# Kernel tuning notes

Measured on AMD Instinct MI355X. Metric: run time of the kernel, lower is better.

## Reference

```python
import jax, jax.numpy as jnp
import numpy as np

NATOMS = 20000
NEDGES = 400000
EMB = 256
NUM_RBF = 50
NUM_GATES = 10
K = 2
FOUT = 128
BASE = 0.0
OUTER = 5.0


def setup_inputs() -> dict:
    key = jax.random.key(0)
    ks = jax.random.split(key, 24)
    z = jax.random.randint(ks[0], (NATOMS,), 0, 100, dtype=jnp.int32)
    pos = jax.random.normal(ks[1], (NATOMS, 3), jnp.float32)
    batch = jnp.zeros((NATOMS,), jnp.int32)
    edge_index = jax.random.randint(ks[2], (2, NEDGES), 0, NATOMS, dtype=jnp.int32)
    edge_weight = jax.random.uniform(ks[3], (NEDGES,), jnp.float32, 0.5, OUTER)
    edge_vec = jax.random.normal(ks[4], (NEDGES, 3), jnp.float32)
    noise = jax.random.normal(ks[5], (NEDGES, NUM_GATES), jnp.float32)
    # learned parameters (torch Linear stored pre-transposed as [in, out])
    emb = jax.random.normal(ks[6], (100, EMB), jnp.float32) * 0.1
    Wd = jax.random.normal(ks[7], (NUM_RBF, EMB), jnp.float32) * 0.05
    bd = jnp.zeros((EMB,), jnp.float32)
    Wdt = jax.random.normal(ks[8], (EMB, EMB), jnp.float32) * 0.05
    bdt = jnp.zeros((EMB,), jnp.float32)
    Wai = jax.random.normal(ks[9], (EMB, EMB), jnp.float32) * 0.05
    bai = jnp.zeros((EMB,), jnp.float32)
    Waj = jax.random.normal(ks[10], (EMB, EMB), jnp.float32) * 0.05
    baj = jnp.zeros((EMB,), jnp.float32)
    Wgam = jax.random.normal(ks[11], (3 * EMB, EMB), jnp.float32) * 0.03
    bgam = jnp.zeros((EMB,), jnp.float32)
    W_g = jax.random.normal(ks[12], (EMB, NUM_GATES), jnp.float32) * 0.01
    W_noise = jax.random.normal(ks[13], (EMB, NUM_GATES), jnp.float32) * 0.01
    W_exp = jax.random.normal(ks[14], (K, EMB, FOUT), jnp.float32) * 0.05
    b_exp = jnp.zeros((K, FOUT), jnp.float32)
    return dict(z=z, pos=pos, batch=batch, edge_index=edge_index,
                edge_weight=edge_weight, edge_vec=edge_vec, noise=noise,
                emb=emb, Wd=Wd, bd=bd, Wdt=Wdt, bdt=bdt, Wai=Wai, bai=bai,
                Waj=Waj, baj=baj, Wgam=Wgam, bgam=bgam, W_g=W_g,
                W_noise=W_noise, W_exp=W_exp, b_exp=b_exp)


def reference(z, pos, batch, edge_index, edge_weight, edge_vec, noise,
              emb, Wd, bd, Wdt, bdt, Wai, bai, Waj, baj, Wgam, bgam,
              W_g, W_noise, W_exp, b_exp):
    n_atoms = z.shape[0]
    src, dst = edge_index[0], edge_index[1]
    x = emb[z]                                              # [N, EMB]
    # Gaussian RBF expansion on [BASE, OUTER]
    offset = jnp.linspace(BASE, OUTER, NUM_RBF)
    coeff = -0.5 / (offset[1] - offset[0]) ** 2
    edge_attr = jnp.exp(coeff * (edge_weight[:, None] - offset) ** 2)  # [E, NUM_RBF]
    # Cosine cutoff (lower cutoff == 0 branch)
    C = 0.5 * (jnp.cos(edge_weight * (np.pi / OUTER)) + 1.0) * (edge_weight < OUTER)
    # normalized edge directions
    evn = edge_vec / jnp.linalg.norm(edge_vec, axis=1, keepdims=True)  # [E, 3]
    d_proj = (edge_attr @ Wd + bd) * C[:, None]             # [E, EMB]
    d_t = d_proj @ Wdt + bdt                                # [E, EMB]
    a_i = x[src] @ Wai + bai                                # [E, EMB]
    a_j = x[dst] @ Waj + baj                                # [E, EMB]
    gamma = jnp.concatenate([d_t, a_i, a_j], axis=1) @ Wgam + bgam  # [E, EMB]
    # noisy top-k gating
    H = d_t @ W_g + noise * jax.nn.softplus(d_t @ W_noise)  # [E, G]
    top_v, top_i = jax.lax.top_k(H, K)                      # [E, K]
    Hm = jnp.where(H >= top_v[:, -1:], H, -jnp.inf)
    gating = jax.nn.softmax(Hm, axis=-1)                    # [E, G]
    # quirk of the original: expert slot i always sees gamma, experts 0..K-1 used
    expert_out = jnp.einsum('ed,kdf->ekf', gamma, W_exp) + b_exp  # [E, K, FOUT]
    gate_w = jnp.take_along_axis(gating, top_i, axis=1)     # [E, K]
    edge_out = (expert_out * gate_w[:, :, None]).sum(axis=1)  # [E, FOUT]
    atom_out = jax.ops.segment_sum(edge_out, src, num_segments=n_atoms)  # [N, FOUT]
    vec = jax.ops.segment_sum(evn[:, :, None] * edge_out[:, None, :], src,
                              num_segments=n_atoms)         # [N, 3, FOUT]
    return atom_out, vec
```

## Files before the change

### kernel.cpp

```cpp
#include <hip/hip_runtime.h>
#include <math.h>

#define NATOMS 20000
#define NEDGES 400000
#define EMBD   256
#define NRBF   50
#define NGATE  10
#define FOUT   128
#define APB    4
#define OUTERC 5.0f

#define RBF_D    (5.0f/49.0f)
#define RBF_INVD (49.0f/5.0f)
#define RBF_C2   (-0.5f*(49.0f/5.0f)*(49.0f/5.0f)*1.4426950408889634f)
#define PI_OVER_OUTER 0.62831853071795864769f

static __device__ __forceinline__ float softplusf(float x){
    return (x > 15.0f) ? x : __logf(1.0f + __expf(x));
}
static __device__ __forceinline__ unsigned bfr(float v){
    unsigned u = __float_as_uint(v);
    return (u + 0x7fffu + ((u >> 16) & 1u)) & 0xffff0000u;
}
#define BLO(u) __uint_as_float((u) << 16)
#define BHI(u) __uint_as_float((u) & 0xffff0000u)

__global__ __launch_bounds__(256) void k_ag(
    const float* __restrict__ Wd, const float* __restrict__ Wdt,
    const float* __restrict__ bd, const float* __restrict__ bdt,
    const float* __restrict__ bgam, const float* __restrict__ Wgam,
    const float* __restrict__ Wexp, const float* __restrict__ bexp,
    const float* __restrict__ Wg, const float* __restrict__ Wn,
    const float* __restrict__ emb,
    const float* __restrict__ Wai, const float* __restrict__ bai,
    const float* __restrict__ Waj, const float* __restrict__ baj,
    const int* __restrict__ esrc, int* __restrict__ counts,
    float* __restrict__ R0, float* __restrict__ R1,
    float* __restrict__ Qg, float* __restrict__ Qn, float* __restrict__ sv,
    float* __restrict__ Ti0, float* __restrict__ Ti1,
    float* __restrict__ Tj0, float* __restrict__ Tj1)
{
    const int b = blockIdx.x, t = threadIdx.x;
    if (b >= 252) {
        int e = (b - 252) * 256 + t;
        if (e < NEDGES) atomicAdd(&counts[esrc[e]], 1);
        return;
    }
    __shared__ float ya[256], za[256];
    if (b >= 52) {
        const int side = (b >= 152);
        const int m = side ? b - 152 : b - 52;
        const float* er = emb + m*EMBD;
        const float* W1 = side ? Waj : Wai;
        const float* b1 = side ? baj : bai;
        float s = b1[t];
        #pragma unroll 8
        for (int k = 0; k < EMBD; k++) s += er[k] * W1[k*EMBD + t];
        ya[t] = s;
        __syncthreads();
        const float* G = Wgam + (size_t)(side ? 512 : 256) * EMBD;
        s = 0.f;
        #pragma unroll 8
        for (int k = 0; k < EMBD; k++) s += ya[k] * G[k*EMBD + t];
        za[t] = s;
        __syncthreads();
        const int half = t >> 7, ff = t & 127;
        const float* WX = Wexp + (size_t)half*EMBD*FOUT;
        s = 0.f;
        #pragma unroll 8
        for (int k = 0; k < EMBD; k++) s += za[k] * WX[k*FOUT + ff];
        float* dst = side ? (half ? Tj1 : Tj0) : (half ? Ti1 : Ti0);
        dst[m*FOUT + ff] = s;
        return;
    }
    const int m = b;
    float s;
    if (m < 50) {
        const float* wr = Wd + m*EMBD;
        s = 0.f;
        #pragma unroll 8
        for (int k = 0; k < EMBD; k++) s += wr[k] * Wdt[k*EMBD + t];
    } else if (m == 50) {
        s = 0.f;
        #pragma unroll 8
        for (int k = 0; k < EMBD; k++) s += bd[k] * Wdt[k*EMBD + t];
    } else {
        s = bdt[t];
    }
    ya[t] = s;
    __syncthreads();
    s = 0.f;
    #pragma unroll 8
    for (int k = 0; k < EMBD; k++) s += ya[k] * Wgam[k*EMBD + t];
    if (m == 51) s += bgam[t];
    za[t] = s;
    __syncthreads();
    const int half = t >> 7, ff = t & 127;
    const float* WX = Wexp + (size_t)half*EMBD*FOUT;
    s = 0.f;
    #pragma unroll 8
    for (int k = 0; k < EMBD; k++) s += za[k] * WX[k*FOUT + ff];
    if (m < 50)       (half ? R1 : R0)[m*FOUT + ff] = s;
    else if (m == 50) sv[half*FOUT + ff] = s;
    else              sv[256 + half*FOUT + ff] = s + bexp[half*FOUT + ff];
    if (t < 20) {
        const int tt = t % 10;
        const float* WT = (t < 10) ? Wg : Wn;
        float q = 0.f;
        #pragma unroll 8
        for (int k = 0; k < EMBD; k++) q += ya[k] * WT[k*NGATE + tt];
        if (m < 50) { float* Q = (t < 10) ? Qg : Qn; Q[m*12 + tt] = q; }
        else {
            int off = (m == 50) ? ((t < 10) ? 512 : 532) : ((t < 10) ? 522 : 542);
            sv[off + tt] = q;
            float* Q = (t < 10) ? Qg : Qn; Q[m*12 + tt] = 0.f;
        }
    }
}

__global__ __launch_bounds__(256) void k_scan(
    const int* __restrict__ counts, int* __restrict__ cursors)
{
    const int t = threadIdx.x;
    __shared__ int part[256];
    const int CH = (NATOMS + 255) / 256;
    int base = t * CH, s = 0;
    for (int i = 0; i < CH; i++) { int idx = base + i; if (idx < NATOMS) s += counts[idx]; }
    part[t] = s;
    __syncthreads();
    for (int d = 1; d < 256; d <<= 1) {
        int v = (t >= d) ? part[t - d] : 0;
        __syncthreads();
        part[t] += v;
        __syncthreads();
    }
    int run = (t == 0) ? 0 : part[t - 1];
    for (int i = 0; i < CH; i++) {
        int idx = base + i;
        if (idx < NATOMS) { cursors[idx] = run; run += counts[idx]; }
    }
}

__global__ __launch_bounds__(256) void k_edge(
    const int* __restrict__ z, const int* __restrict__ esrc, const int* __restrict__ edst,
    const float* __restrict__ ew, const float* __restrict__ evec, const float* __restrict__ noise,
    const float* __restrict__ Qg, const float* __restrict__ Qn, const float* __restrict__ sv,
    int* __restrict__ cursors,
    float4* __restrict__ rec, unsigned* __restrict__ zdj)
{
    __shared__ float qgL[52*12], qnL[52*12];
    __shared__ float nbuf[256*11];
    __shared__ float vbuf[768];
    const int t = threadIdx.x;
    const int e0 = blockIdx.x * 256;

    for (int i = t; i < 52*12; i += 256) { qgL[i] = Qg[i]; qnL[i] = Qn[i]; }
    #pragma unroll
    for (int q = 0; q < 10; q++) {
        int idx = q*256 + t; long long g = (long long)e0*10 + idx;
        if (g < (long long)NEDGES*10) { int r_ = idx/10; nbuf[r_*11 + (idx - r_*10)] = noise[g]; }
    }
    #pragma unroll
    for (int q = 0; q < 3; q++) {
        int idx = q*256 + t; long long g = (long long)e0*3 + idx;
        if (g < (long long)NEDGES*3) vbuf[idx] = evec[g];
    }
    __syncthreads();

    int e = e0 + t;
    if (e >= NEDGES) return;
    float w = ew[e];
    float C = (w < OUTERC) ? 0.5f*(__cosf(w*PI_OVER_OUTER) + 1.0f) : 0.0f;
    int iw = (int)(w * RBF_INVD);
    int j0 = (iw - 4) & ~3;
    j0 = max(0, min(40, j0));
    float rW[12];
    #pragma unroll
    for (int k = 0; k < 12; k++) { float tt = w - (j0+k)*RBF_D; rW[k] = exp2f(RBF_C2*tt*tt); }
    float hg[NGATE], hn[NGATE];
    #pragma unroll
    for (int g2 = 0; g2 < NGATE; g2++) { hg[g2] = 0.f; hn[g2] = 0.f; }
    #pragma unroll
    for (int k = 0; k < 12; k++) {
        float rk = rW[k];
        const float* qg = &qgL[(j0+k)*12];
        const float* qn = &qnL[(j0+k)*12];
        float4 ga = *(const float4*)qg; float4 gb = *(const float4*)(qg+4);
        float2 gc = *(const float2*)(qg+8);
        float4 na = *(const float4*)qn; float4 nb = *(const float4*)(qn+4);
        float2 nc = *(const float2*)(qn+8);
        hg[0]=fmaf(rk,ga.x,hg[0]); hg[1]=fmaf(rk,ga.y,hg[1]); hg[2]=fmaf(rk,ga.z,hg[2]); hg[3]=fmaf(rk,ga.w,hg[3]);
        hg[4]=fmaf(rk,gb.x,hg[4]); hg[5]=fmaf(rk,gb.y,hg[5]); hg[6]=fmaf(rk,gb.z,hg[6]); hg[7]=fmaf(rk,gb.w,hg[7]);
        hg[8]=fmaf(rk,gc.x,hg[8]); hg[9]=fmaf(rk,gc.y,hg[9]);
        hn[0]=fmaf(rk,na.x,hn[0]); hn[1]=fmaf(rk,na.y,hn[1]); hn[2]=fmaf(rk,na.z,hn[2]); hn[3]=fmaf(rk,na.w,hn[3]);
        hn[4]=fmaf(rk,nb.x,hn[4]); hn[5]=fmaf(rk,nb.y,hn[5]); hn[6]=fmaf(rk,nb.z,hn[6]); hn[7]=fmaf(rk,nb.w,hn[7]);
        hn[8]=fmaf(rk,nc.x,hn[8]); hn[9]=fmaf(rk,nc.y,hn[9]);
    }
    float H[NGATE];
    #pragma unroll
    for (int g2 = 0; g2 < NGATE; g2++) {
        float gv = C*(hg[g2] + sv[512+g2]) + sv[522+g2];
        float nv = C*(hn[g2] + sv[532+g2]) + sv[542+g2];
        H[g2] = gv + nbuf[t*11 + g2] * softplusf(nv);
    }
    float m1 = -INFINITY, m2 = -INFINITY;
    #pragma unroll
    for (int g2 = 0; g2 < NGATE; g2++) {
        float v = H[g2];
        if (v > m1) { m2 = m1; m1 = v; } else if (v > m2) { m2 = v; }
    }
    float den = 0.f;
    #pragma unroll
    for (int g2 = 0; g2 < NGATE; g2++) den += (H[g2] >= m2) ? __expf(H[g2] - m1) : 0.f;
    float inv = 1.0f / den;
    float g0 = inv;
    float g1 = __expf(m2 - m1) * inv;

    float ex = vbuf[t*3+0], ey = vbuf[t*3+1], ez = vbuf[t*3+2];
    float rn = rsqrtf(ex*ex + ey*ey + ez*ez);
    ex *= rn; ey *= rn; ez *= rn;
    int zd = z[edst[e]];
    int p = atomicAdd(&cursors[esrc[e]], 1);

    rec[p] = make_float4(w,
        __uint_as_float((bfr(g0)>>16) | bfr(g1)),
        __uint_as_float((bfr(ex)>>16) | bfr(ey)),
        __uint_as_float(bfr(ez)));
    zdj[p] = (unsigned)zd | (__float2uint_rn(C * 16777215.0f) << 7);
}

#define FFLUSH() { \
    accS[aCur-aBeg][pair][f] = make_float4(accA, accX, accY, accZ); \
    accA=accX=accY=accZ=0.f; \
    aCur++; \
    if (aCur < aEnd) { nextEnd = neNxt; int an_ = aCur + 1; if (an_ < aEnd) neNxt = cursors[an_]; } \
    else nextEnd = 0x7fffffff; }

#define FCOMP(GI, D, TJ) { \
    int gi = (GI); \
    while (gi == nextEnd) FFLUSH() \
    unsigned gu = __float_as_uint(D.y), xu = __float_as_uint(D.z), eu = __float_as_uint(D.w); \
    float u_ = (pair ? BHI(gu) : BLO(gu)) * (TJ); \
    accA += u_; \
    accX = fmaf(BLO(xu), u_, accX); \
    accY = fmaf(BHI(xu), u_, accY); \
    accZ = fmaf(BHI(eu), u_, accZ); }

#define SFLUSH() { \
    int aIdx_ = aCur - aBeg; \
    if (sAct) { \
        *(float4*)&Plds[0][l][aIdx_*4] = make_float4(p00,p10,p20,p30); \
        *(float4*)&Plds[1][l][aIdx_*4] = make_float4(p01,p11,p21,p31); \
        p00=p01=p10=p11=p20=p21=p30=p31=0.f; } \
    aCur++; \
    if (aCur < aEnd) { nextEnd = neNxt; int an_ = aCur + 1; if (an_ < aEnd) neNxt = cursors[an_]; } \
    else nextEnd = 0x7fffffff; }

#define SCOMP(GI, D, CZ) { \
    int gi = (GI); \
    while (gi == nextEnd) SFLUSH() \
    unsigned gu = __float_as_uint(D.y), xu = __float_as_uint(D.z), eu = __float_as_uint(D.w); \
    float g0f = BLO(gu), g1f = BHI(gu); \
    float exf = BLO(xu), eyf = BHI(xu), ezf = BHI(eu); \
    float Cc_ = __uint2float_rn((CZ) >> 7) * (1.0f/16777215.0f); \
    float t_ = D.x - sjf; \
    float e2_ = exp2f(RBF_C2*t_*t_); \
    float b_ = isG ? Cc_*e2_ : (isC ? Cc_ : 1.0f); \
    float bg0 = b_*g0f, bg1 = b_*g1f; \
    p00 += bg0; p01 += bg1; \
    p10 = fmaf(exf,bg0,p10); p11 = fmaf(exf,bg1,p11); \
    p20 = fmaf(eyf,bg0,p20); p21 = fmaf(eyf,bg1,p21); \
    p30 = fmaf(ezf,bg0,p30); p31 = fmaf(ezf,bg1,p31); }

#define DOT16(PA,PB,PC,PD,R_) { \
    D00=fmaf(PA.x,R_,D00); D01=fmaf(PA.y,R_,D01); D02=fmaf(PA.z,R_,D02); D03=fmaf(PA.w,R_,D03); \
    D10=fmaf(PB.x,R_,D10); D11=fmaf(PB.y,R_,D11); D12=fmaf(PB.z,R_,D12); D13=fmaf(PB.w,R_,D13); \
    D20=fmaf(PC.x,R_,D20); D21=fmaf(PC.y,R_,D21); D22=fmaf(PC.z,R_,D22); D23=fmaf(PC.w,R_,D23); \
    D30=fmaf(PD.x,R_,D30); D31=fmaf(PD.y,R_,D31); D32=fmaf(PD.z,R_,D32); D33=fmaf(PD.w,R_,D33); }

__global__ __launch_bounds__(320) void k_main(
    const int* __restrict__ z, const int* __restrict__ cursors,
    const float4* __restrict__ rec, const unsigned* __restrict__ zdj,
    const float* __restrict__ R0, const float* __restrict__ R1,
    const float* __restrict__ Ti0, const float* __restrict__ Ti1,
    const float* __restrict__ Tj0, const float* __restrict__ Tj1,
    const float* __restrict__ sv, float* __restrict__ out)
{
    __shared__ float4 accS[APB][2][FOUT];
    __shared__ __align__(16) float Plds[2][52][20];
    const int tid = threadIdx.x;

    const int aBeg = blockIdx.x * APB, aEnd = aBeg + APB;
    const int eBeg = aBeg ? cursors[aBeg-1] : 0;
    const int eEnd = cursors[aEnd-1];

    int aCur = aBeg;
    int nextEnd = cursors[aCur];
    int neNxt = (aBeg+1 < aEnd) ? cursors[aBeg+1] : 0x7fffffff;

    const int pair = (tid >> 7) & 1, f = tid & 127;

    if (tid < 256) {
        const float* TjT = pair ? Tj1 : Tj0;
        float accA=0.f, accX=0.f, accY=0.f, accZ=0.f;

        float4 c0 = rec[eBeg],   c1 = rec[eBeg+1];
        float4 d0 = rec[eBeg+2], d1 = rec[eBeg+3];
        unsigned zj4 = zdj[eBeg+4], zj5 = zdj[eBeg+5];
        float ct0 = TjT[(zdj[eBeg]  & 0x7fu)*FOUT + f];
        float ct1 = TjT[(zdj[eBeg+1]& 0x7fu)*FOUT + f];
        float dt0 = TjT[(zdj[eBeg+2]& 0x7fu)*FOUT + f];
        float dt1 = TjT[(zdj[eBeg+3]& 0x7fu)*FOUT + f];

        for (int i = eBeg; i < eEnd; i += 2) {
            float4 e0 = rec[i+4], e1 = rec[i+5];
            unsigned zj6 = zdj[i+6], zj7 = zdj[i+7];
            float et0 = TjT[(zj4 & 0x7fu)*FOUT + f];
            float et1 = TjT[(zj5 & 0x7fu)*FOUT + f];

            FCOMP(i,   c0, ct0)
            if (i + 1 < eEnd) { FCOMP(i+1, c1, ct1) }

            c0 = d0; c1 = d1; d0 = e0; d1 = e1;
            ct0 = dt0; ct1 = dt1; dt0 = et0; dt1 = et1;
            zj4 = zj6; zj5 = zj7;
        }
        while (aCur < aEnd) FFLUSH();
    } else {
        const int l = tid - 256;
        const bool sAct = (l < 52);
        const bool isG = (l < 50), isC = (l == 50);
        const float sjf = l * RBF_D;
        float p00=0,p01=0,p10=0,p11=0,p20=0,p21=0,p30=0,p31=0;

        float4 c0 = rec[eBeg],   c1 = rec[eBeg+1];
        float4 d0 = rec[eBeg+2], d1 = rec[eBeg+3];
        unsigned z0 = zdj[eBeg],   z1 = zdj[eBeg+1];
        unsigned z2 = zdj[eBeg+2], z3 = zdj[eBeg+3];

        for (int i = eBeg; i < eEnd; i += 2) {
            float4 e0 = rec[i+4], e1 = rec[i+5];
            unsigned z4 = zdj[i+4], z5 = zdj[i+5];

            SCOMP(i,   c0, z0)
            if (i + 1 < eEnd) { SCOMP(i+1, c1, z1) }

            c0 = d0; c1 = d1; d0 = e0; d1 = e1;
            z0 = z2; z1 = z3; z2 = z4; z3 = z5;
        }
        while (aCur < aEnd) SFLUSH();
    }
    __syncthreads();

    if (tid < 256) {
        const float* Rtab = pair ? R1 : R0;
        const float* TiT  = pair ? Ti1 : Ti0;
        const float sVv = sv[pair*FOUT + f];
        const float dVv = sv[256 + pair*FOUT + f];
        float D00=0,D01=0,D02=0,D03=0, D10=0,D11=0,D12=0,D13=0;
        float D20=0,D21=0,D22=0,D23=0, D30=0,D31=0,D32=0,D33=0;
        #pragma unroll 5
        for (int j = 0; j < 50; j++) {
            float r = Rtab[j*FOUT + f];
            const float* pb = &Plds[pair][j][0];
            float4 qa = *(const float4*)(pb+0);
            float4 qb = *(const float4*)(pb+4);
            float4 qc = *(const float4*)(pb+8);
            float4 qd = *(const float4*)(pb+12);
            DOT16(qa, qb, qc, qd, r)
        }
        {
            const float* pb = &Plds[pair][50][0];
            float4 qa = *(const float4*)(pb+0);
            float4 qb = *(const float4*)(pb+4);
            float4 qc = *(const float4*)(pb+8);
            float4 qd = *(const float4*)(pb+12);
            DOT16(qa, qb, qc, qd, sVv)
        }
        {
            const float* pb = &Plds[pair][51][0];
            float4 qa = *(const float4*)(pb+0);
            float4 qb = *(const float4*)(pb+4);
            float4 qc = *(const float4*)(pb+8);
            float4 qd = *(const float4*)(pb+12);
            float r0 = dVv + TiT[z[aBeg+0]*FOUT + f];
            float r1 = dVv + TiT[z[aBeg+1]*FOUT + f];
            float r2 = dVv + TiT[z[aBeg+2]*FOUT + f];
            float r3 = dVv + TiT[z[aBeg+3]*FOUT + f];
            D00=fmaf(qa.x,r0,D00); D01=fmaf(qa.y,r0,D01); D02=fmaf(qa.z,r0,D02); D03=fmaf(qa.w,r0,D03);
            D10=fmaf(qb.x,r1,D10); D11=fmaf(qb.y,r1,D11); D12=fmaf(qb.z,r1,D12); D13=fmaf(qb.w,r1,D13);
            D20=fmaf(qc.x,r2,D20); D21=fmaf(qc.y,r2,D21); D22=fmaf(qc.z,r2,D22); D23=fmaf(qc.w,r2,D23);
            D30=fmaf(qd.x,r3,D30); D31=fmaf(qd.y,r3,D31); D32=fmaf(qd.z,r3,D32); D33=fmaf(qd.w,r3,D33);
        }
        float4 t;
        t = accS[0][pair][f]; t.x+=D00; t.y+=D01; t.z+=D02; t.w+=D03; accS[0][pair][f] = t;
        t = accS[1][pair][f]; t.x+=D10; t.y+=D11; t.z+=D12; t.w+=D13; accS[1][pair][f] = t;
        t = accS[2][pair][f]; t.x+=D20; t.y+=D21; t.z+=D22; t.w+=D23; accS[2][pair][f] = t;
        t = accS[3][pair][f]; t.x+=D30; t.y+=D31; t.z+=D32; t.w+=D33; accS[3][pair][f] = t;
    }
    __syncthreads();
    if (tid < FOUT) {
        #pragma unroll
        for (int a2 = 0; a2 < APB; a2++) {
            float4 v0 = accS[a2][0][tid];
            float4 v1 = accS[a2][1][tid];
            int atom = aBeg + a2;
            out[(size_t)atom*FOUT + tid] = v0.x + v1.x;
            float* vb = out + (size_t)NATOMS*FOUT + (size_t)atom*3*FOUT;
            vb[tid]        = v0.y + v1.y;
            vb[FOUT+tid]   = v0.z + v1.z;
            vb[2*FOUT+tid] = v0.w + v1.w;
        }
    }
}

extern "C" void kernel_launch(void* const* d_in, const int* in_sizes, int n_in,
                              void* d_out, int out_size, void* d_ws, size_t ws_size,
                              hipStream_t stream)
{
    const int*   z    = (const int*)d_in[0];
    const int*   ei   = (const int*)d_in[3];
    const int*   esrc = ei;
    const int*   edst = ei + NEDGES;
    const float* ew   = (const float*)d_in[4];
    const float* evec = (const float*)d_in[5];
    const float* nz   = (const float*)d_in[6];
    const float* emb  = (const float*)d_in[7];
    const float* Wd   = (const float*)d_in[8];
    const float* bd   = (const float*)d_in[9];
    const float* Wdt  = (const float*)d_in[10];
    const float* bdt  = (const float*)d_in[11];
    const float* Wai  = (const float*)d_in[12];
    const float* bai  = (const float*)d_in[13];
    const float* Waj  = (const float*)d_in[14];
    const float* baj  = (const float*)d_in[15];
    const float* Wgam = (const float*)d_in[16];
    const float* bgam = (const float*)d_in[17];
    const float* Wg   = (const float*)d_in[18];
    const float* Wn   = (const float*)d_in[19];
    const float* Wexp = (const float*)d_in[20];
    const float* bexp = (const float*)d_in[21];
    float* out = (float*)d_out;

    char* w = (char*)d_ws;
    auto alloc = [&](size_t bytes) -> void* {
        void* p = (void*)w;
        w += (bytes + 255) & ~(size_t)255;
        return p;
    };
    int*   counts  = (int*)alloc(NATOMS * 4);
    int*   cursors = (int*)alloc(NATOMS * 4);
    float* R0  = (float*)alloc(NRBF*FOUT*4);
    float* R1  = (float*)alloc(NRBF*FOUT*4);
    float* Qg  = (float*)alloc(52*12*4);
    float* Qn  = (float*)alloc(52*12*4);
    float* Ti0 = (float*)alloc(100*FOUT*4);
    float* Ti1 = (float*)alloc(100*FOUT*4);
    float* Tj0 = (float*)alloc(100*FOUT*4);
    float* Tj1 = (float*)alloc(100*FOUT*4);
    float* sv  = (float*)alloc(552*4);
    float4*   rec = (float4*)alloc(((size_t)NEDGES + 16)*16);
    unsigned* zdj = (unsigned*)alloc(((size_t)NEDGES + 16)*4);

    hipMemsetAsync(counts, 0, NATOMS*4, stream);
    hipMemsetAsync(rec + NEDGES, 0, 16*sizeof(float4), stream);
    hipMemsetAsync(zdj + NEDGES, 0, 16*4, stream);

    {
        int grid = 252 + (NEDGES + 255) / 256;
        k_ag<<<grid, 256, 0, stream>>>(Wd, Wdt, bd, bdt, bgam, Wgam, Wexp, bexp,
                                       Wg, Wn, emb, Wai, bai, Waj, baj,
                                       esrc, counts, R0, R1, Qg, Qn, sv,
                                       Ti0, Ti1, Tj0, Tj1);
    }
    k_scan<<<1, 256, 0, stream>>>(counts, cursors);
    {
        int grid = (NEDGES + 255) / 256;
        k_edge<<<grid, 256, 0, stream>>>(z, esrc, edst, ew, evec, nz,
                                         Qg, Qn, sv, cursors, rec, zdj);
    }
    {
        int grid = NATOMS / APB;
        k_main<<<grid, 320, 0, stream>>>(z, cursors, rec, zdj,
                                         R0, R1, Ti0, Ti1, Tj0, Tj1, sv, out);
    }
}
```

Measured before the change: 406.0 us.

## Bin per-edge Tj gathers into per-element histograms and split edge scan across all waves

Stops gathering the Tj table per edge per output feature. Each block instead builds a small shared-memory histogram indexed by destination element type (gate weight times unit-vector components) using LDS atomics, then contracts it with the Tj table over the 100 element types. The edge scan for the RBF moments is now split across all five wavefronts with LDS atomic accumulation, replacing the earlier split of 256 feature threads and one RBF wave. This trades per-edge global gathers for LDS atomics, extra zero-initialisation and a fixed 100-row contraction per block.

```diff
diff --git a/kernel.cpp b/kernel.cpp
--- a/kernel.cpp
+++ b/kernel.cpp
@@ -229,54 +229,21 @@
     zdj[p] = (unsigned)zd | (__float2uint_rn(C * 16777215.0f) << 7);
 }
 
-#define FFLUSH() { \
-    accS[aCur-aBeg][pair][f] = make_float4(accA, accX, accY, accZ); \
-    accA=accX=accY=accZ=0.f; \
-    aCur++; \
-    if (aCur < aEnd) { nextEnd = neNxt; int an_ = aCur + 1; if (an_ < aEnd) neNxt = cursors[an_]; } \
-    else nextEnd = 0x7fffffff; }
-
-#define FCOMP(GI, D, TJ) { \
-    int gi = (GI); \
-    while (gi == nextEnd) FFLUSH() \
-    unsigned gu = __float_as_uint(D.y), xu = __float_as_uint(D.z), eu = __float_as_uint(D.w); \
-    float u_ = (pair ? BHI(gu) : BLO(gu)) * (TJ); \
-    accA += u_; \
-    accX = fmaf(BLO(xu), u_, accX); \
-    accY = fmaf(BHI(xu), u_, accY); \
-    accZ = fmaf(BHI(eu), u_, accZ); }
-
-#define SFLUSH() { \
-    int aIdx_ = aCur - aBeg; \
-    if (sAct) { \
-        *(float4*)&Plds[0][l][aIdx_*4] = make_float4(p00,p10,p20,p30); \
-        *(float4*)&Plds[1][l][aIdx_*4] = make_float4(p01,p11,p21,p31); \
-        p00=p01=p10=p11=p20=p21=p30=p31=0.f; } \
-    aCur++; \
-    if (aCur < aEnd) { nextEnd = neNxt; int an_ = aCur + 1; if (an_ < aEnd) neNxt = cursors[an_]; } \
-    else nextEnd = 0x7fffffff; }
-
-#define SCOMP(GI, D, CZ) { \
-    int gi = (GI); \
-    while (gi == nextEnd) SFLUSH() \
-    unsigned gu = __float_as_uint(D.y), xu = __float_as_uint(D.z), eu = __float_as_uint(D.w); \
-    float g0f = BLO(gu), g1f = BHI(gu); \
-    float exf = BLO(xu), eyf = BHI(xu), ezf = BHI(eu); \
-    float Cc_ = __uint2float_rn((CZ) >> 7) * (1.0f/16777215.0f); \
-    float t_ = D.x - sjf; \
-    float e2_ = exp2f(RBF_C2*t_*t_); \
-    float b_ = isG ? Cc_*e2_ : (isC ? Cc_ : 1.0f); \
-    float bg0 = b_*g0f, bg1 = b_*g1f; \
-    p00 += bg0; p01 += bg1; \
-    p10 = fmaf(exf,bg0,p10); p11 = fmaf(exf,bg1,p11); \
-    p20 = fmaf(eyf,bg0,p20); p21 = fmaf(eyf,bg1,p21); \
-    p30 = fmaf(ezf,bg0,p30); p31 = fmaf(ezf,bg1,p31); }
-
 #define DOT16(PA,PB,PC,PD,R_) { \
     D00=fmaf(PA.x,R_,D00); D01=fmaf(PA.y,R_,D01); D02=fmaf(PA.z,R_,D02); D03=fmaf(PA.w,R_,D03); \
     D10=fmaf(PB.x,R_,D10); D11=fmaf(PB.y,R_,D11); D12=fmaf(PB.z,R_,D12); D13=fmaf(PB.w,R_,D13); \
     D20=fmaf(PC.x,R_,D20); D21=fmaf(PC.y,R_,D21); D22=fmaf(PC.z,R_,D22); D23=fmaf(PC.w,R_,D23); \
     D30=fmaf(PD.x,R_,D30); D31=fmaf(PD.y,R_,D31); D32=fmaf(PD.z,R_,D32); D33=fmaf(PD.w,R_,D33); }
+
+#define PDUMP() { \
+    if (sAct) { \
+        atomicAdd(&Plds[0][l][aIdx*4+0], p00); atomicAdd(&Plds[0][l][aIdx*4+1], p10); \
+        atomicAdd(&Plds[0][l][aIdx*4+2], p20); atomicAdd(&Plds[0][l][aIdx*4+3], p30); \
+        atomicAdd(&Plds[1][l][aIdx*4+0], p01); atomicAdd(&Plds[1][l][aIdx*4+1], p11); \
+        atomicAdd(&Plds[1][l][aIdx*4+2], p21); atomicAdd(&Plds[1][l][aIdx*4+3], p31); \
+        p00=p01=p10=p11=p20=p21=p30=p31=0.f; } \
+    aIdx++; \
+    nextEnd = (aIdx==1)?end2:(aIdx==2)?end3:(aIdx==3)?eEnd:0x7fffffff; }
 
 __global__ __launch_bounds__(320) void k_main(
     const int* __restrict__ z, const int* __restrict__ cursors,
@@ -286,79 +253,66 @@
     const float* __restrict__ Tj0, const float* __restrict__ Tj1,
     const float* __restrict__ sv, float* __restrict__ out)
 {
-    __shared__ float4 accS[APB][2][FOUT];
     __shared__ __align__(16) float Plds[2][52][20];
+    __shared__ __align__(16) float Hlds[2][100][16];
+    __shared__ float redS[APB][4][FOUT];
     const int tid = threadIdx.x;
-
-    const int aBeg = blockIdx.x * APB, aEnd = aBeg + APB;
+    const int wv = tid >> 6, l = tid & 63;
+
+    for (int i = tid; i < 2*52*20; i += 320) ((float*)Plds)[i] = 0.f;
+    for (int i = tid; i < 2*100*16; i += 320) ((float*)Hlds)[i] = 0.f;
+    __syncthreads();
+
+    const int aBeg = blockIdx.x * APB;
     const int eBeg = aBeg ? cursors[aBeg-1] : 0;
-    const int eEnd = cursors[aEnd-1];
-
-    int aCur = aBeg;
-    int nextEnd = cursors[aCur];
-    int neNxt = (aBeg+1 < aEnd) ? cursors[aBeg+1] : 0x7fffffff;
-
-    const int pair = (tid >> 7) & 1, f = tid & 127;
-
-    if (tid < 256) {
-        const float* TjT = pair ? Tj1 : Tj0;
-        float accA=0.f, accX=0.f, accY=0.f, accZ=0.f;
-
-        float4 c0 = rec[eBeg],   c1 = rec[eBeg+1];
-        float4 d0 = rec[eBeg+2], d1 = rec[eBeg+3];
-        unsigned zj4 = zdj[eBeg+4], zj5 = zdj[eBeg+5];
-        float ct0 = TjT[(zdj[eBeg]  & 0x7fu)*FOUT + f];
-        float ct1 = TjT[(zdj[eBeg+1]& 0x7fu)*FOUT + f];
-        float dt0 = TjT[(zdj[eBeg+2]& 0x7fu)*FOUT + f];
-        float dt1 = TjT[(zdj[eBeg+3]& 0x7fu)*FOUT + f];
-
-        for (int i = eBeg; i < eEnd; i += 2) {
-            float4 e0 = rec[i+4], e1 = rec[i+5];
-            unsigned zj6 = zdj[i+6], zj7 = zdj[i+7];
-            float et0 = TjT[(zj4 & 0x7fu)*FOUT + f];
-            float et1 = TjT[(zj5 & 0x7fu)*FOUT + f];
-
-            FCOMP(i,   c0, ct0)
-            if (i + 1 < eEnd) { FCOMP(i+1, c1, ct1) }
-
-            c0 = d0; c1 = d1; d0 = e0; d1 = e1;
-            ct0 = dt0; ct1 = dt1; dt0 = et0; dt1 = et1;
-            zj4 = zj6; zj5 = zj7;
-        }
-        while (aCur < aEnd) FFLUSH();
-    } else {
-        const int l = tid - 256;
+    const int end1 = cursors[aBeg],   end2 = cursors[aBeg+1];
+    const int end3 = cursors[aBeg+2], eEnd = cursors[aBeg+3];
+
+    {
         const bool sAct = (l < 52);
         const bool isG = (l < 50), isC = (l == 50);
         const float sjf = l * RBF_D;
+        const bool hAct = (l >= 52) && (l < 60);
+        const int hh = (l - 52) >> 2, hv = (l - 52) & 3;
         float p00=0,p01=0,p10=0,p11=0,p20=0,p21=0,p30=0,p31=0;
-
-        float4 c0 = rec[eBeg],   c1 = rec[eBeg+1];
-        float4 d0 = rec[eBeg+2], d1 = rec[eBeg+3];
-        unsigned z0 = zdj[eBeg],   z1 = zdj[eBeg+1];
-        unsigned z2 = zdj[eBeg+2], z3 = zdj[eBeg+3];
-
-        for (int i = eBeg; i < eEnd; i += 2) {
-            float4 e0 = rec[i+4], e1 = rec[i+5];
-            unsigned z4 = zdj[i+4], z5 = zdj[i+5];
-
-            SCOMP(i,   c0, z0)
-            if (i + 1 < eEnd) { SCOMP(i+1, c1, z1) }
-
-            c0 = d0; c1 = d1; d0 = e0; d1 = e1;
-            z0 = z2; z1 = z3; z2 = z4; z3 = z5;
-        }
-        while (aCur < aEnd) SFLUSH();
-    }
-    __syncthreads();
-
+        int aIdx = 0;
+        int nextEnd = end1;
+
+        for (int i = eBeg + wv; i < eEnd; i += 5) {
+            while (i >= nextEnd) PDUMP()
+            float4 r = rec[i];
+            unsigned zz = zdj[i];
+            unsigned gu = __float_as_uint(r.y), xu = __float_as_uint(r.z), eu = __float_as_uint(r.w);
+            float g0f = BLO(gu), g1f = BHI(gu);
+            float exf = BLO(xu), eyf = BHI(xu), ezf = BHI(eu);
+            float Cc = __uint2float_rn(zz >> 7) * (1.0f/16777215.0f);
+            float t_ = r.x - sjf;
+            float e2 = exp2f(RBF_C2*t_*t_);
+            float b_ = isG ? Cc*e2 : (isC ? Cc : 1.0f);
+            float bg0 = b_*g0f, bg1 = b_*g1f;
+            p00 += bg0; p01 += bg1;
+            p10 = fmaf(exf,bg0,p10); p11 = fmaf(exf,bg1,p11);
+            p20 = fmaf(eyf,bg0,p20); p21 = fmaf(eyf,bg1,p21);
+            p30 = fmaf(ezf,bg0,p30); p31 = fmaf(ezf,bg1,p31);
+            if (hAct) {
+                int zd = (int)(zz & 0x7fu);
+                float uv = (hv==0) ? 1.0f : ((hv==1) ? exf : ((hv==2) ? eyf : ezf));
+                atomicAdd(&Hlds[hh][zd][aIdx*4+hv], uv * (hh ? g1f : g0f));
+            }
+        }
+        while (aIdx < APB) PDUMP()
+    }
+    __syncthreads();
+
+    const int pair = (tid >> 7) & 1, f = tid & 127;
+    float D00=0,D01=0,D02=0,D03=0, D10=0,D11=0,D12=0,D13=0;
+    float D20=0,D21=0,D22=0,D23=0, D30=0,D31=0,D32=0,D33=0;
     if (tid < 256) {
         const float* Rtab = pair ? R1 : R0;
         const float* TiT  = pair ? Ti1 : Ti0;
+        const float* TjT  = pair ? Tj1 : Tj0;
         const float sVv = sv[pair*FOUT + f];
         const float dVv = sv[256 + pair*FOUT + f];
-        float D00=0,D01=0,D02=0,D03=0, D10=0,D11=0,D12=0,D13=0;
-        float D20=0,D21=0,D22=0,D23=0, D30=0,D31=0,D32=0,D33=0;
         #pragma unroll 5
         for (int j = 0; j < 50; j++) {
             float r = Rtab[j*FOUT + f];
@@ -392,25 +346,42 @@
             D20=fmaf(qc.x,r2,D20); D21=fmaf(qc.y,r2,D21); D22=fmaf(qc.z,r2,D22); D23=fmaf(qc.w,r2,D23);
             D30=fmaf(qd.x,r3,D30); D31=fmaf(qd.y,r3,D31); D32=fmaf(qd.z,r3,D32); D33=fmaf(qd.w,r3,D33);
         }
-        float4 t;
-        t = accS[0][pair][f]; t.x+=D00; t.y+=D01; t.z+=D02; t.w+=D03; accS[0][pair][f] = t;
-        t = accS[1][pair][f]; t.x+=D10; t.y+=D11; t.z+=D12; t.w+=D13; accS[1][pair][f] = t;
-        t = accS[2][pair][f]; t.x+=D20; t.y+=D21; t.z+=D22; t.w+=D23; accS[2][pair][f] = t;
-        t = accS[3][pair][f]; t.x+=D30; t.y+=D31; t.z+=D32; t.w+=D33; accS[3][pair][f] = t;
-    }
-    __syncthreads();
-    if (tid < FOUT) {
-        #pragma unroll
-        for (int a2 = 0; a2 < APB; a2++) {
-            float4 v0 = accS[a2][0][tid];
-            float4 v1 = accS[a2][1][tid];
-            int atom = aBeg + a2;
-            out[(size_t)atom*FOUT + tid] = v0.x + v1.x;
-            float* vb = out + (size_t)NATOMS*FOUT + (size_t)atom*3*FOUT;
-            vb[tid]        = v0.y + v1.y;
-            vb[FOUT+tid]   = v0.z + v1.z;
-            vb[2*FOUT+tid] = v0.w + v1.w;
-        }
+        #pragma unroll 4
+        for (int zd = 0; zd < 100; zd++) {
+            float r = TjT[zd*FOUT + f];
+            const float* pb = &Hlds[pair][zd][0];
+            float4 qa = *(const float4*)(pb+0);
+            float4 qb = *(const float4*)(pb+4);
+            float4 qc = *(const float4*)(pb+8);
+            float4 qd = *(const float4*)(pb+12);
+            DOT16(qa, qb, qc, qd, r)
+        }
+    }
+    if (tid < 256 && pair == 1) {
+        redS[0][0][f]=D00; redS[0][1][f]=D01; redS[0][2][f]=D02; redS[0][3][f]=D03;
+        redS[1][0][f]=D10; redS[1][1][f]=D11; redS[1][2][f]=D12; redS[1][3][f]=D13;
+        redS[2][0][f]=D20; redS[2][1][f]=D21; redS[2][2][f]=D22; redS[2][3][f]=D23;
+        redS[3][0][f]=D30; redS[3][1][f]=D31; redS[3][2][f]=D32; redS[3][3][f]=D33;
+    }
+    __syncthreads();
+    if (tid < 256 && pair == 0) {
+        float* vb = out + (size_t)NATOMS*FOUT + (size_t)aBeg*3*FOUT;
+        out[(size_t)(aBeg+0)*FOUT + f] = D00 + redS[0][0][f];
+        vb[0*3*FOUT + f]        = D01 + redS[0][1][f];
+        vb[0*3*FOUT + FOUT+f]   = D02 + redS[0][2][f];
+        vb[0*3*FOUT + 2*FOUT+f] = D03 + redS[0][3][f];
+        out[(size_t)(aBeg+1)*FOUT + f] = D10 + redS[1][0][f];
+        vb[1*3*FOUT + f]        = D11 + redS[1][1][f];
+        vb[1*3*FOUT + FOUT+f]   = D12 + redS[1][2][f];
+        vb[1*3*FOUT + 2*FOUT+f] = D13 + redS[1][3][f];
+        out[(size_t)(aBeg+2)*FOUT + f] = D20 + redS[2][0][f];
+        vb[2*3*FOUT + f]        = D21 + redS[2][1][f];
+        vb[2*3*FOUT + FOUT+f]   = D22 + redS[2][2][f];
+        vb[2*3*FOUT + 2*FOUT+f] = D23 + redS[2][3][f];
+        out[(size_t)(aBeg+3)*FOUT + f] = D30 + redS[3][0][f];
+        vb[3*3*FOUT + f]        = D31 + redS[3][1][f];
+        vb[3*3*FOUT + FOUT+f]   = D32 + redS[3][2][f];
+        vb[3*3*FOUT + 2*FOUT+f] = D33 + redS[3][3][f];
     }
 }
 
```

After: 646.2 us. 59.2% more time.
